# Performance work log

Hardware: AMD Instinct MI355X
Metric: run time of the kernel (lower is better)

Reference implementation:

```python
import jax, jax.numpy as jnp
import numpy as np

C_IN = 2048
C_HID = 256

def _co_attention(query_features, reference_features, Wq, bq, Wk, bk):
    # 1x1 conv == channel-mixing matmul. Wq/Wk: (hid, C_in)
    Q = jnp.einsum('bchw,oc->bohw', query_features, Wq) + bq[None, :, None, None]
    K = jnp.einsum('bchw,oc->bohw', reference_features, Wk) + bk[None, :, None, None]
    b, c, h2, w2 = reference_features.shape
    p = h2 * w2
    Kf = K.reshape(b, C_HID, p)                      # (b, hid, p)
    V = reference_features.reshape(b, c, p)          # (b, C_in, p)
    # scores: bcij,bckl->bijkl flattened over (kl) -> (b, h1, w1, p)
    scores = jnp.einsum('bchw,bcp->bhwp', Q, Kf)
    attn = jax.nn.softmax(scores, axis=-1)
    # attended: bijp,bcp->bcij
    attended = jnp.einsum('bhwp,bcp->bchw', attn, V)
    return attended

def setup_inputs() -> dict:
    key = jax.random.key(0)
    ks = jax.random.split(key, 10)
    b, h, w = 8, 32, 32
    scale = 1.0 / np.sqrt(C_IN)
    return {
        'feature_1': jax.random.normal(ks[0], (b, C_IN, h, w), jnp.float32),
        'feature_2': jax.random.normal(ks[1], (b, C_IN, h, w), jnp.float32),
        'Wq1': jax.random.normal(ks[2], (C_HID, C_IN), jnp.float32) * scale,
        'bq1': jnp.zeros((C_HID,), jnp.float32),
        'Wk1': jax.random.normal(ks[3], (C_HID, C_IN), jnp.float32) * scale,
        'bk1': jnp.zeros((C_HID,), jnp.float32),
        'Wq2': jax.random.normal(ks[4], (C_HID, C_IN), jnp.float32) * scale,
        'bq2': jnp.zeros((C_HID,), jnp.float32),
        'Wk2': jax.random.normal(ks[5], (C_HID, C_IN), jnp.float32) * scale,
        'bk2': jnp.zeros((C_HID,), jnp.float32),
    }

def reference(feature_1, feature_2, Wq1, bq1, Wk1, bk1, Wq2, bq2, Wk2, bk2):
    x1 = _co_attention(feature_1, feature_2, Wq1, bq1, Wk1, bk1)
    x2 = _co_attention(feature_2, feature_1, Wq2, bq2, Wk2, bk2)
    return (x1, x2)
```

## Files before the change

### kernel.cpp

```cpp
#include <hip/hip_runtime.h>
#include <math.h>

#define NB   8
#define CIN  2048
#define CHID 256
#define NP   1024

typedef _Float16 f16;
typedef _Float16 f16x8 __attribute__((ext_vector_type(8)));
typedef float    f32x4 __attribute__((ext_vector_type(4)));


__device__ inline void stage_f16(const f16* __restrict__ g, int stride,
                                 int outer0, int k0, f16* lds, int t)
{
    const int r0 = t >> 3;
    const int sl = t & 7;
#pragma unroll
    for (int it = 0; it < 4; ++it) {
        const int row = r0 + it * 32;
        const int4 v = *reinterpret_cast<const int4*>(
            &g[(size_t)(outer0 + row) * stride + k0 + sl * 8]);
        const int byte = (row * 128 + sl * 16) ^ ((row & 7) << 4);
        *reinterpret_cast<int4*>(reinterpret_cast<char*>(lds) + byte) = v;
    }
}

__device__ inline f16x8 ldsfrag(const f16* lds, int row, int kbyte)
{
    const char* p = reinterpret_cast<const char*>(lds) +
                    ((row * 128 + kbyte) ^ ((row & 7) << 4));
    return *reinterpret_cast<const f16x8*>(p);
}

__global__ __launch_bounds__(256) void convert_W(
    const float* __restrict__ Wq1, const float* __restrict__ Wk1,
    const float* __restrict__ Wq2, const float* __restrict__ Wk2,
    f16* __restrict__ Wf)
{
    const int n4 = CHID * CIN / 4;
    const int i = blockIdx.x * 256 + threadIdx.x;
    const int mat = i / n4;
    const int j = i - mat * n4;
    const float* W = (mat == 0) ? Wq1 : (mat == 1) ? Wk1 : (mat == 2) ? Wq2 : Wk2;
    const float4 v = *reinterpret_cast<const float4*>(&W[(size_t)j * 4]);
    union { f16 h[4]; uint2 u; } o;
    o.h[0] = (f16)v.x; o.h[1] = (f16)v.y; o.h[2] = (f16)v.z; o.h[3] = (f16)v.w;
    *reinterpret_cast<uint2*>(&Wf[(size_t)i * 4]) = o.u;
}

__global__ __launch_bounds__(256) void convert_F(
    const float* __restrict__ f1, const float* __restrict__ f2,
    f16* __restrict__ Ft)
{
    const int z = blockIdx.z;
    const int feat = z >> 3, b = z & 7;
    const float* F = (feat ? f2 : f1) + (size_t)b * CIN * NP;
    f16* T = Ft + ((size_t)feat * NB + b) * NP * CIN;
    const int c0 = blockIdx.y * 64, p0 = blockIdx.x * 64;

    __shared__ float tile[64][65];
    const int t = threadIdx.x;
    const int r = t >> 4, c4 = (t & 15) * 4;

#pragma unroll
    for (int it = 0; it < 4; ++it) {
        const int cr = r + it * 16;
        const float4 v = *reinterpret_cast<const float4*>(
            &F[(size_t)(c0 + cr) * NP + p0 + c4]);
        tile[cr][c4 + 0] = v.x;
        tile[cr][c4 + 1] = v.y;
        tile[cr][c4 + 2] = v.z;
        tile[cr][c4 + 3] = v.w;
    }
    __syncthreads();
#pragma unroll
    for (int it = 0; it < 4; ++it) {
        const int pr = r + it * 16;
        union { f16 h[4]; uint2 u; } o;
        o.h[0] = (f16)tile[c4 + 0][pr];
        o.h[1] = (f16)tile[c4 + 1][pr];
        o.h[2] = (f16)tile[c4 + 2][pr];
        o.h[3] = (f16)tile[c4 + 3][pr];
        *reinterpret_cast<uint2*>(&T[(size_t)(p0 + pr) * CIN + c0 + c4]) = o.u;
    }
}

__global__ __launch_bounds__(256) void proj_mfma(
    const f16* __restrict__ Wf, const f16* __restrict__ Ft,
    const float* __restrict__ bq1, const float* __restrict__ bk1,
    const float* __restrict__ bq2, const float* __restrict__ bk2,
    f16* __restrict__ QK)
{
    const int bid = blockIdx.x;
    const int b = bid & 7;
    const int within = bid >> 3;
    const int tile = within & 15;
    const int mat_in_pair = (within >> 4) & 1;
    const int pairsel = within >> 5;
    const int mat = pairsel == 0 ? (mat_in_pair ? 3 : 0)
                                 : (mat_in_pair ? 2 : 1);

    const f16* A = Wf + (size_t)mat * CHID * CIN;
    const int feat = (mat == 0 || mat == 3) ? 0 : 1;
    const f16* B = Ft + ((size_t)feat * NB + b) * NP * CIN;
    const float* bias = (mat == 0) ? bq1 : (mat == 1) ? bk1 : (mat == 2) ? bq2 : bk2;
    f16* C = QK + ((size_t)mat * NB + b) * NP * CHID;

    const int m0 = (tile >> 3) * 128;
    const int n0 = (tile & 7) * 128;

    __shared__ __align__(16) f16 As[128 * 64];
    __shared__ __align__(16) f16 Bs[128 * 64];

    const int t = threadIdx.x, lane = t & 63, w = t >> 6;
    const int wm = w >> 1, wn = w & 1;

    f32x4 acc[4][4];
#pragma unroll
    for (int i = 0; i < 4; ++i)
#pragma unroll
        for (int j = 0; j < 4; ++j) acc[i][j] = (f32x4){0.f, 0.f, 0.f, 0.f};

    for (int k0 = 0; k0 < CIN; k0 += 64) {
        stage_f16(A, CIN, m0, k0, As, t);
        stage_f16(B, CIN, n0, k0, Bs, t);
        __syncthreads();
#pragma unroll
        for (int kh = 0; kh < 2; ++kh) {
            f16x8 a[4], bb[4];
#pragma unroll
            for (int fm = 0; fm < 4; ++fm)
                a[fm] = ldsfrag(As, wm * 64 + fm * 16 + (lane & 15),
                                kh * 64 + (lane >> 4) * 16);
#pragma unroll
            for (int fn = 0; fn < 4; ++fn)
                bb[fn] = ldsfrag(Bs, wn * 64 + fn * 16 + (lane & 15),
                                 kh * 64 + (lane >> 4) * 16);
#pragma unroll
            for (int fm = 0; fm < 4; ++fm)
#pragma unroll
                for (int fn = 0; fn < 4; ++fn)
                    acc[fm][fn] = __builtin_amdgcn_mfma_f32_16x16x32_f16(
                        a[fm], bb[fn], acc[fm][fn], 0, 0, 0);
        }
        __syncthreads();
    }

    const int lo4 = (lane >> 4) * 4, lp = lane & 15;
#pragma unroll
    for (int fm = 0; fm < 4; ++fm) {
        const int obase = m0 + wm * 64 + fm * 16 + lo4;
        const float4 b4 = *reinterpret_cast<const float4*>(&bias[obase]);
#pragma unroll
        for (int fn = 0; fn < 4; ++fn) {
            const int p = n0 + wn * 64 + fn * 16 + lp;
            union { f16 h[4]; uint2 u; } o;
            o.h[0] = (f16)(acc[fm][fn][0] + b4.x);
            o.h[1] = (f16)(acc[fm][fn][1] + b4.y);
            o.h[2] = (f16)(acc[fm][fn][2] + b4.z);
            o.h[3] = (f16)(acc[fm][fn][3] + b4.w);
            *reinterpret_cast<uint2*>(&C[(size_t)p * CHID + obase]) = o.u;
        }
    }
}

__global__ __launch_bounds__(256) void scores_mfma(
    const f16* __restrict__ QK, float* __restrict__ S, int side)
{
    const int bid = blockIdx.x;
    const int b = bid & 7;
    const int tile = bid >> 3;
    const f16* A = QK + ((size_t)(side * 2 + 0) * NB + b) * NP * CHID;
    const f16* B = QK + ((size_t)(side * 2 + 1) * NB + b) * NP * CHID;
    float* Sb = S + (size_t)b * NP * NP;

    const int m0 = (tile >> 3) * 128;
    const int n0 = (tile & 7) * 128;

    __shared__ __align__(16) f16 As[128 * 64];
    __shared__ __align__(16) f16 Bs[128 * 64];

    const int t = threadIdx.x, lane = t & 63, w = t >> 6;
    const int wm = w >> 1, wn = w & 1;

    f32x4 acc[4][4];
#pragma unroll
    for (int i = 0; i < 4; ++i)
#pragma unroll
        for (int j = 0; j < 4; ++j) acc[i][j] = (f32x4){0.f, 0.f, 0.f, 0.f};

    for (int k0 = 0; k0 < CHID; k0 += 64) {
        stage_f16(A, CHID, m0, k0, As, t);
        stage_f16(B, CHID, n0, k0, Bs, t);
        __syncthreads();
#pragma unroll
        for (int kh = 0; kh < 2; ++kh) {
            f16x8 a[4], bb[4];
#pragma unroll
            for (int fm = 0; fm < 4; ++fm)
                a[fm] = ldsfrag(As, wm * 64 + fm * 16 + (lane & 15),
                                kh * 64 + (lane >> 4) * 16);
#pragma unroll
            for (int fn = 0; fn < 4; ++fn)
                bb[fn] = ldsfrag(Bs, wn * 64 + fn * 16 + (lane & 15),
                                 kh * 64 + (lane >> 4) * 16);
#pragma unroll
            for (int fm = 0; fm < 4; ++fm)
#pragma unroll
                for (int fn = 0; fn < 4; ++fn)
                    acc[fm][fn] = __builtin_amdgcn_mfma_f32_16x16x32_f16(
                        a[fm], bb[fn], acc[fm][fn], 0, 0, 0);
        }
        __syncthreads();
    }

    const int lo4 = (lane >> 4) * 4, lp = lane & 15;
#pragma unroll
    for (int fm = 0; fm < 4; ++fm) {
#pragma unroll
        for (int fn = 0; fn < 4; ++fn) {
            const int q = m0 + wm * 64 + fm * 16 + lo4;
            const int p = n0 + wn * 64 + fn * 16 + lp;
#pragma unroll
            for (int r = 0; r < 4; ++r)
                Sb[(size_t)(q + r) * NP + p] = acc[fm][fn][r];
        }
    }
}

__global__ __launch_bounds__(256) void softmax_rows(
    const float* __restrict__ S, f16* __restrict__ attn)
{
    const size_t row = blockIdx.x;
    const float* Sr = S + row * NP;
    f16* Ar = attn + row * NP;
    const int t = threadIdx.x;

    const float4 v = *reinterpret_cast<const float4*>(&Sr[t * 4]);
    float m = fmaxf(fmaxf(v.x, v.y), fmaxf(v.z, v.w));
#pragma unroll
    for (int off = 32; off; off >>= 1) m = fmaxf(m, __shfl_xor(m, off));
    __shared__ float redm[4], reds[4];
    if ((t & 63) == 0) redm[t >> 6] = m;
    __syncthreads();
    m = fmaxf(fmaxf(redm[0], redm[1]), fmaxf(redm[2], redm[3]));

    float4 e;
    e.x = __expf(v.x - m); e.y = __expf(v.y - m);
    e.z = __expf(v.z - m); e.w = __expf(v.w - m);
    float s = e.x + e.y + e.z + e.w;
#pragma unroll
    for (int off = 32; off; off >>= 1) s += __shfl_xor(s, off);
    if ((t & 63) == 0) reds[t >> 6] = s;
    __syncthreads();
    const float inv = 1.0f / (reds[0] + reds[1] + reds[2] + reds[3]);

    union { f16 h[4]; uint2 u; } o;
    o.h[0] = (f16)(e.x * inv); o.h[1] = (f16)(e.y * inv);
    o.h[2] = (f16)(e.z * inv); o.h[3] = (f16)(e.w * inv);
    *reinterpret_cast<uint2*>(&Ar[t * 4]) = o.u;
}

__global__ __launch_bounds__(256) void attended_mfma(
    const float* __restrict__ V, const f16* __restrict__ attn,
    float* __restrict__ out)
{
    const int bid = blockIdx.x;
    const int b = bid & 7;
    const int tile = bid >> 3;
    const int qt = tile & 7;
    const int ct = tile >> 3;

    const float* Vb = V + (size_t)b * CIN * NP;
    const f16* Ab = attn + (size_t)b * NP * NP;
    float* Ob = out + (size_t)b * CIN * NP;

    const int m0 = ct * 128;
    const int n0 = qt * 128;

    __shared__ __align__(16) f16 As[128 * 64];
    __shared__ __align__(16) f16 Bs[128 * 64];

    const int t = threadIdx.x, lane = t & 63, w = t >> 6;
    const int wm = w >> 1, wn = w & 1;

    f32x4 acc[4][4];
#pragma unroll
    for (int i = 0; i < 4; ++i)
#pragma unroll
        for (int j = 0; j < 4; ++j) acc[i][j] = (f32x4){0.f, 0.f, 0.f, 0.f};

    const int r0 = t >> 3, sl = t & 7;

    for (int k0 = 0; k0 < NP; k0 += 64) {
#pragma unroll
        for (int it = 0; it < 4; ++it) {
            const int row = r0 + it * 32;
            const float* src = &Vb[(size_t)(m0 + row) * NP + k0 + sl * 8];
            const float4 v0 = *reinterpret_cast<const float4*>(src);
            const float4 v1 = *reinterpret_cast<const float4*>(src + 4);
            union { f16 h[8]; int4 i4; } pk;
            pk.h[0] = (f16)v0.x; pk.h[1] = (f16)v0.y;
            pk.h[2] = (f16)v0.z; pk.h[3] = (f16)v0.w;
            pk.h[4] = (f16)v1.x; pk.h[5] = (f16)v1.y;
            pk.h[6] = (f16)v1.z; pk.h[7] = (f16)v1.w;
            const int byte = (row * 128 + sl * 16) ^ ((row & 7) << 4);
            *reinterpret_cast<int4*>(reinterpret_cast<char*>(As) + byte) = pk.i4;
        }
        stage_f16(Ab, NP, n0, k0, Bs, t);
        __syncthreads();
#pragma unroll
        for (int kh = 0; kh < 2; ++kh) {
            f16x8 a[4], bb[4];
#pragma unroll
            for (int fm = 0; fm < 4; ++fm)
                a[fm] = ldsfrag(As, wm * 64 + fm * 16 + (lane & 15),
                                kh * 64 + (lane >> 4) * 16);
#pragma unroll
            for (int fn = 0; fn < 4; ++fn)
                bb[fn] = ldsfrag(Bs, wn * 64 + fn * 16 + (lane & 15),
                                 kh * 64 + (lane >> 4) * 16);
#pragma unroll
            for (int fm = 0; fm < 4; ++fm)
#pragma unroll
                for (int fn = 0; fn < 4; ++fn)
                    acc[fm][fn] = __builtin_amdgcn_mfma_f32_16x16x32_f16(
                        a[fm], bb[fn], acc[fm][fn], 0, 0, 0);
        }
        __syncthreads();
    }

    const int lo4 = (lane >> 4) * 4, lp = lane & 15;
#pragma unroll
    for (int fm = 0; fm < 4; ++fm) {
#pragma unroll
        for (int fn = 0; fn < 4; ++fn) {
            const int c = m0 + wm * 64 + fm * 16 + lo4;
            const int q = n0 + wn * 64 + fn * 16 + lp;
#pragma unroll
            for (int r = 0; r < 4; ++r)
                Ob[(size_t)(c + r) * NP + q] = acc[fm][fn][r];
        }
    }
}

extern "C" void kernel_launch(void* const* d_in, const int* in_sizes, int n_in,
                              void* d_out, int out_size, void* d_ws, size_t ws_size,
                              hipStream_t stream)
{
    const float* f1  = (const float*)d_in[0];
    const float* f2  = (const float*)d_in[1];
    const float* Wq1 = (const float*)d_in[2];
    const float* bq1 = (const float*)d_in[3];
    const float* Wk1 = (const float*)d_in[4];
    const float* bk1 = (const float*)d_in[5];
    const float* Wq2 = (const float*)d_in[6];
    const float* bq2 = (const float*)d_in[7];
    const float* Wk2 = (const float*)d_in[8];
    const float* bk2 = (const float*)d_in[9];
    float* out = (float*)d_out;

    char* ws = (char*)d_ws;
    f16*   Ft   = (f16*)ws;
    float* S    = (float*)ws;
    f16*   attn = (f16*)(ws + 33554432);
    f16*   QK   = (f16*)(ws + 67108864);
    f16*   Wf   = (f16*)(ws + 83886080);

    const dim3 blk(256);

    convert_W<<<dim3(4 * CHID * CIN / 4 / 256), blk, 0, stream>>>(
        Wq1, Wk1, Wq2, Wk2, Wf);
    convert_F<<<dim3(NP / 64, CIN / 64, 2 * NB), blk, 0, stream>>>(f1, f2, Ft);

    proj_mfma<<<dim3(512), blk, 0, stream>>>(
        Wf, Ft, bq1, bk1, bq2, bk2, QK);

    for (int side = 0; side < 2; ++side) {
        scores_mfma<<<dim3(512), blk, 0, stream>>>(QK, S, side);
        softmax_rows<<<dim3(NB * NP), blk, 0, stream>>>(S, attn);
        const float* V = (side == 0) ? f2 : f1;
        float* o = out + (size_t)side * NB * CIN * NP;
        attended_mfma<<<dim3(1024), blk, 0, stream>>>(V, attn, o);
    }
}
```

Baseline: 462.9 us.

## Stage GEMM tiles with direct global-to-LDS loads and pre-converted fp16 V

Replaces the register-staged global->LDS tile copies in all three MFMA GEMMs with buffer/global_load_lds direct transfers. The XOR swizzle moves from the LDS address to the source column selection, so the fragment read layout stays the same. convert_F now also writes an fp16 copy of the features in channel-major layout. attended_mfma then loads fp16 V directly instead of reading fp32 and converting inside every tile loop, which halves V read traffic there. The cost is an extra fp16 write of both feature tensors plus additional workspace.

```diff
diff --git a/kernel.cpp b/kernel.cpp
--- a/kernel.cpp
+++ b/kernel.cpp
@@ -10,19 +10,24 @@
 typedef _Float16 f16x8 __attribute__((ext_vector_type(8)));
 typedef float    f32x4 __attribute__((ext_vector_type(4)));
 
-
-__device__ inline void stage_f16(const f16* __restrict__ g, int stride,
-                                 int outer0, int k0, f16* lds, int t)
-{
-    const int r0 = t >> 3;
-    const int sl = t & 7;
+typedef const __attribute__((address_space(1))) void GAS;
+typedef __attribute__((address_space(3))) void LAS;
+
+
+__device__ inline void stage_gl(const f16* __restrict__ g, int stride,
+                                int outer0, int k0, f16* lds, int t)
+{
+    const int lane = t & 63, w = t >> 6;
+    const int r8 = lane >> 3;
+    const int xsl = (lane & 7) ^ r8;
 #pragma unroll
     for (int it = 0; it < 4; ++it) {
-        const int row = r0 + it * 32;
-        const int4 v = *reinterpret_cast<const int4*>(
-            &g[(size_t)(outer0 + row) * stride + k0 + sl * 8]);
-        const int byte = (row * 128 + sl * 16) ^ ((row & 7) << 4);
-        *reinterpret_cast<int4*>(reinterpret_cast<char*>(lds) + byte) = v;
+        const int chunk = w * 4 + it;
+        const int row = chunk * 8 + r8;
+        const f16* src = &g[(size_t)(outer0 + row) * stride + k0 + xsl * 8];
+        __builtin_amdgcn_global_load_lds(
+            (GAS*)src, (LAS*)(reinterpret_cast<char*>(lds) + chunk * 1024),
+            16, 0, 0);
     }
 }
 
@@ -51,12 +56,13 @@
 
 __global__ __launch_bounds__(256) void convert_F(
     const float* __restrict__ f1, const float* __restrict__ f2,
-    f16* __restrict__ Ft)
+    f16* __restrict__ Ft, f16* __restrict__ Vf)
 {
     const int z = blockIdx.z;
     const int feat = z >> 3, b = z & 7;
     const float* F = (feat ? f2 : f1) + (size_t)b * CIN * NP;
     f16* T = Ft + ((size_t)feat * NB + b) * NP * CIN;
+    f16* Vb = Vf + ((size_t)feat * NB + b) * CIN * NP;
     const int c0 = blockIdx.y * 64, p0 = blockIdx.x * 64;
 
     __shared__ float tile[64][65];
@@ -72,6 +78,9 @@
         tile[cr][c4 + 1] = v.y;
         tile[cr][c4 + 2] = v.z;
         tile[cr][c4 + 3] = v.w;
+        union { f16 h[4]; uint2 u; } s;
+        s.h[0] = (f16)v.x; s.h[1] = (f16)v.y; s.h[2] = (f16)v.z; s.h[3] = (f16)v.w;
+        *reinterpret_cast<uint2*>(&Vb[(size_t)(c0 + cr) * NP + p0 + c4]) = s.u;
     }
     __syncthreads();
 #pragma unroll
@@ -123,8 +132,8 @@
         for (int j = 0; j < 4; ++j) acc[i][j] = (f32x4){0.f, 0.f, 0.f, 0.f};
 
     for (int k0 = 0; k0 < CIN; k0 += 64) {
-        stage_f16(A, CIN, m0, k0, As, t);
-        stage_f16(B, CIN, n0, k0, Bs, t);
+        stage_gl(A, CIN, m0, k0, As, t);
+        stage_gl(B, CIN, n0, k0, Bs, t);
         __syncthreads();
 #pragma unroll
         for (int kh = 0; kh < 2; ++kh) {
@@ -191,8 +200,8 @@
         for (int j = 0; j < 4; ++j) acc[i][j] = (f32x4){0.f, 0.f, 0.f, 0.f};
 
     for (int k0 = 0; k0 < CHID; k0 += 64) {
-        stage_f16(A, CHID, m0, k0, As, t);
-        stage_f16(B, CHID, n0, k0, Bs, t);
+        stage_gl(A, CHID, m0, k0, As, t);
+        stage_gl(B, CHID, n0, k0, Bs, t);
         __syncthreads();
 #pragma unroll
         for (int kh = 0; kh < 2; ++kh) {
@@ -263,7 +272,7 @@
 }
 
 __global__ __launch_bounds__(256) void attended_mfma(
-    const float* __restrict__ V, const f16* __restrict__ attn,
+    const f16* __restrict__ Vf, const f16* __restrict__ attn,
     float* __restrict__ out)
 {
     const int bid = blockIdx.x;
@@ -272,7 +281,7 @@
     const int qt = tile & 7;
     const int ct = tile >> 3;
 
-    const float* Vb = V + (size_t)b * CIN * NP;
+    const f16* Vb = Vf + (size_t)b * CIN * NP;
     const f16* Ab = attn + (size_t)b * NP * NP;
     float* Ob = out + (size_t)b * CIN * NP;
 
@@ -291,24 +300,9 @@
 #pragma unroll
         for (int j = 0; j < 4; ++j) acc[i][j] = (f32x4){0.f, 0.f, 0.f, 0.f};
 
-    const int r0 = t >> 3, sl = t & 7;
-
     for (int k0 = 0; k0 < NP; k0 += 64) {
-#pragma unroll
-        for (int it = 0; it < 4; ++it) {
-            const int row = r0 + it * 32;
-            const float* src = &Vb[(size_t)(m0 + row) * NP + k0 + sl * 8];
-            const float4 v0 = *reinterpret_cast<const float4*>(src);
-            const float4 v1 = *reinterpret_cast<const float4*>(src + 4);
-            union { f16 h[8]; int4 i4; } pk;
-            pk.h[0] = (f16)v0.x; pk.h[1] = (f16)v0.y;
-            pk.h[2] = (f16)v0.z; pk.h[3] = (f16)v0.w;
-            pk.h[4] = (f16)v1.x; pk.h[5] = (f16)v1.y;
-            pk.h[6] = (f16)v1.z; pk.h[7] = (f16)v1.w;
-            const int byte = (row * 128 + sl * 16) ^ ((row & 7) << 4);
-            *reinterpret_cast<int4*>(reinterpret_cast<char*>(As) + byte) = pk.i4;
-        }
-        stage_f16(Ab, NP, n0, k0, Bs, t);
+        stage_gl(Vb, NP, m0, k0, As, t);
+        stage_gl(Ab, NP, n0, k0, Bs, t);
         __syncthreads();
 #pragma unroll
         for (int kh = 0; kh < 2; ++kh) {
@@ -367,12 +361,13 @@
     f16*   attn = (f16*)(ws + 33554432);
     f16*   QK   = (f16*)(ws + 67108864);
     f16*   Wf   = (f16*)(ws + 83886080);
+    f16*   Vf   = (f16*)(ws + 88080384);
 
     const dim3 blk(256);
 
     convert_W<<<dim3(4 * CHID * CIN / 4 / 256), blk, 0, stream>>>(
         Wq1, Wk1, Wq2, Wk2, Wf);
-    convert_F<<<dim3(NP / 64, CIN / 64, 2 * NB), blk, 0, stream>>>(f1, f2, Ft);
+    convert_F<<<dim3(NP / 64, CIN / 64, 2 * NB), blk, 0, stream>>>(f1, f2, Ft, Vf);
 
     proj_mfma<<<dim3(512), blk, 0, stream>>>(
         Wf, Ft, bq1, bk1, bq2, bk2, QK);
@@ -380,8 +375,8 @@
     for (int side = 0; side < 2; ++side) {
         scores_mfma<<<dim3(512), blk, 0, stream>>>(QK, S, side);
         softmax_rows<<<dim3(NB * NP), blk, 0, stream>>>(S, attn);
-        const float* V = (side == 0) ? f2 : f1;
+        const f16* Vside = Vf + (size_t)(side ^ 1) * NB * CIN * NP;
         float* o = out + (size_t)side * NB * CIN * NP;
-        attended_mfma<<<dim3(1024), blk, 0, stream>>>(V, attn, o);
-    }
-}
+        attended_mfma<<<dim3(1024), blk, 0, stream>>>(Vside, attn, o);
+    }
+}
```

Result: faster. 441.2 us (-4.7%).
